# Kernel tuning notes

Measured on AMD Instinct MI355X. Metric: run time of the kernel, lower is better.

The kernel has to match this reference:

```python
import jax, jax.numpy as jnp
import numpy as np

N, D, E, TOP_K = 4096, 1024, 8, 2
NEG_INF = -1e38


def setup_inputs() -> dict:
    key = jax.random.key(0)
    ks = jax.random.split(key, 6)
    s = 1.0 / np.sqrt(D)
    return {
        "x": jax.random.normal(ks[0], (N, D), jnp.float32),
        "noise": jax.random.normal(ks[1], (E,), jnp.float32),
        "Wg": jax.random.normal(ks[2], (D, E), jnp.float32) * s,
        "Wn": jax.random.normal(ks[3], (D, E), jnp.float32) * s,
        "We": jax.random.normal(ks[4], (E, D, D), jnp.float32) * s,
        "be": jax.random.normal(ks[5], (E, D), jnp.float32) * 0.01,
    }


def reference(x, noise, Wg, Wn, We, be):
    # Gating: H = Wg(x) + randn(E) * softplus(Wnoise(x))   (Eq. 4-5)
    g = x @ Wg                                      # [N, E]
    H = g + noise[None, :] * jax.nn.softplus(x @ Wn)  # [N, E]
    # Keep top_k entries of H, set the rest to -Inf (scatter of bottom E-k)
    vals, idx = jax.lax.top_k(H, TOP_K)             # [N, k]
    keep = jnp.full_like(H, NEG_INF)
    keep = keep.at[jnp.arange(H.shape[0])[:, None], idx].set(vals)
    G = jax.nn.softmax(keep, axis=1)                # [N, E]; masked entries -> 0
    # Expert outputs; masked experts have G==0 so dense weighted sum matches
    # the sparse per-example loop: out_n = sum_j G[n,j] * expert_j(x_n)
    Y = jnp.einsum('nd,edh->neh', x, We) + be[None, :, :]  # [N, E, D]
    out = jnp.einsum('ne,neh->nh', G, Y)            # [N, D]
    return out
```

## Files before the change

### kernel.cpp

```cpp
#include <hip/hip_runtime.h>
#include <hip/hip_bf16.h>
#include <stdint.h>

#define NR   4096
#define DIM  1024
#define NE   8
#define BM   64
#define BN   128
#define BK   64

typedef __attribute__((ext_vector_type(8))) short  bf16x8;
typedef __attribute__((ext_vector_type(8))) ushort u16x8;
typedef __attribute__((ext_vector_type(4))) float  f32x4;

__device__ __forceinline__ ushort f2bf(float f) {
    union { __hip_bfloat16 h; ushort u; } cv;
    cv.h = __float2bfloat16(f);
    return cv.u;
}

__device__ __forceinline__ void gload16(const void* g, void* l) {
    __builtin_amdgcn_global_load_lds(
        (const __attribute__((address_space(1))) unsigned int*)g,
        (__attribute__((address_space(3))) unsigned int*)l, 16, 0, 0);
}

__global__ __launch_bounds__(256)
void k1_prep(const float* __restrict__ Wg, const float* __restrict__ Wn,
             float* __restrict__ WT, float* __restrict__ out) {
    const int tid = threadIdx.x;
    if (blockIdx.x < 8) {
        const int k    = blockIdx.x * 128 + (tid >> 1);
        const int half = tid & 1;
        const float* src = half ? Wn : Wg;
        const float4* s4 = (const float4*)(src + (size_t)k * NE);
        float4 a = s4[0], b = s4[1];
        float* d = WT + (size_t)half * 8 * DIM;
        d[(size_t)0 * DIM + k] = a.x; d[(size_t)1 * DIM + k] = a.y;
        d[(size_t)2 * DIM + k] = a.z; d[(size_t)3 * DIM + k] = a.w;
        d[(size_t)4 * DIM + k] = b.x; d[(size_t)5 * DIM + k] = b.y;
        d[(size_t)6 * DIM + k] = b.z; d[(size_t)7 * DIM + k] = b.w;
    } else {
        const int vb = blockIdx.x - 8;
        float4 z = {0.f, 0.f, 0.f, 0.f};
        for (int i = vb * 256 + tid; i < NR * DIM / 4; i += 512 * 256)
            ((float4*)out)[i] = z;
    }
}

__global__ __launch_bounds__(256)
void k2_main(const float* __restrict__ We, ushort* __restrict__ WeT,
             const float* __restrict__ x, const float* __restrict__ noise,
             const float* __restrict__ WT, ushort* __restrict__ xbf,
             uint32_t* __restrict__ eid, float2* __restrict__ wpair) {
    __shared__ float smem[64 * 68];
    const int tid = threadIdx.x;
    if (blockIdx.x < 2048) {
        const int b  = blockIdx.x;
        const int e  = b >> 8, kt = (b >> 4) & 15, ct = b & 15;
        const float* src = We + ((size_t)e * DIM + (size_t)kt * 64) * DIM + ct * 64;
#pragma unroll
        for (int j = 0; j < 4; ++j) {
            int idx = tid + j * 256;
            int r = idx >> 4, c4 = idx & 15;
            *(float4*)&smem[r * 68 + c4 * 4] = *(const float4*)(src + (size_t)r * DIM + c4 * 4);
        }
        __syncthreads();
        ushort* dst = WeT + ((size_t)e * DIM + (size_t)ct * 64) * DIM + kt * 64;
#pragma unroll
        for (int j = 0; j < 2; ++j) {
            int u = tid + j * 256;
            int c = u >> 3, ch = u & 7;
            ushort tmp[8];
#pragma unroll
            for (int q = 0; q < 8; ++q) tmp[q] = f2bf(smem[(ch * 8 + q) * 68 + c]);
            *(u16x8*)(dst + (size_t)c * DIM + ch * 8) = *(u16x8*)tmp;
        }
    } else {
        const int w = tid >> 6, l = tid & 63;
        const int row = (blockIdx.x - 2048) * 4 + w;
        const float* xr = x + (size_t)row * DIM;

        float4 xv[4];
#pragma unroll
        for (int q = 0; q < 4; ++q) xv[q] = *(const float4*)(xr + q * 256 + l * 4);
#pragma unroll
        for (int q = 0; q < 4; ++q) {
            ushort4 xb;
            xb.x = f2bf(xv[q].x); xb.y = f2bf(xv[q].y);
            xb.z = f2bf(xv[q].z); xb.w = f2bf(xv[q].w);
            *(ushort4*)(xbf + (size_t)row * DIM + q * 256 + l * 4) = xb;
        }

        float acc[16];
#pragma unroll
        for (int u = 0; u < 16; ++u) {
            const float* wr_ = WT + (size_t)u * DIM + l * 4;
            float s = 0.f;
#pragma unroll
            for (int q = 0; q < 4; ++q) {
                float4 wv = *(const float4*)(wr_ + q * 256);
                s += xv[q].x * wv.x + xv[q].y * wv.y + xv[q].z * wv.z + xv[q].w * wv.w;
            }
            acc[u] = s;
        }
#pragma unroll
        for (int u = 0; u < 16; ++u) smem[(w * 64 + l) * 17 + u] = acc[u];
        asm volatile("s_waitcnt lgkmcnt(0)" ::: "memory");
        const int c = l >> 4, u = l & 15;
        float v = 0.f;
#pragma unroll
        for (int i = 0; i < 16; ++i) v += smem[(w * 64 + c * 16 + i) * 17 + u];
        v += __shfl_xor(v, 16, 64);
        v += __shfl_xor(v, 32, 64);

        const int e = l & 7;
        float ag = __shfl(v, e, 64);
        float an = __shfl(v, e + 8, 64);
        float sp = (an > 0.f) ? (an + log1pf(expf(-an))) : log1pf(expf(an));
        float H  = ag + noise[e] * sp;

        float Hh[8];
#pragma unroll
        for (int k = 0; k < 8; ++k) Hh[k] = __shfl(H, k, 64);
        if (l == 0) {
            int e0 = 0; float v0 = Hh[0];
#pragma unroll
            for (int k = 1; k < 8; ++k) if (Hh[k] > v0) { v0 = Hh[k]; e0 = k; }
            int e1 = -1; float v1 = 0.f;
#pragma unroll
            for (int k = 0; k < 8; ++k)
                if (k != e0 && (e1 < 0 || Hh[k] > v1)) { v1 = Hh[k]; e1 = k; }
            float rr = expf(v1 - v0);
            float w0 = 1.f / (1.f + rr), w1 = 1.f - w0;
            eid[row] = (uint32_t)e0 | ((uint32_t)e1 << 8);
            float2 wp; wp.x = w0; wp.y = w1;
            wpair[row] = wp;
        }
    }
}

__global__ __launch_bounds__(1024)
void bucket_build(const uint32_t* __restrict__ eid, const float2* __restrict__ wpair,
                  int* __restrict__ cnt, int* __restrict__ idxl, float* __restrict__ wl) {
    const int bucket = blockIdx.x;
    const int slot = bucket >> 3, ex = bucket & 7;
    __shared__ int base;
    __shared__ int wsum[16];
    if (threadIdx.x == 0) base = 0;
    const int wid = threadIdx.x >> 6, lane = threadIdx.x & 63;
    int* bidx = idxl + (size_t)bucket * NR;
    float* bwl = wl + (size_t)bucket * NR;

    for (int c0 = 0; c0 < NR; c0 += 1024) {
        const int row = c0 + threadIdx.x;
        const uint32_t em = eid[row];
        const int e = slot ? (int)((em >> 8) & 255u) : (int)(em & 255u);
        const bool m = (e == ex);
        const unsigned long long bal = __ballot(m);
        if (lane == 0) wsum[wid] = __popcll(bal);
        __syncthreads();
        int wbase = base;
        for (int i = 0; i < wid; ++i) wbase += wsum[i];
        const int pos = wbase + __popcll(bal & ((1ull << lane) - 1ull));
        if (m) {
            bidx[pos] = row;
            float2 wp = wpair[row];
            bwl[pos]  = slot ? wp.y : wp.x;
        }
        __syncthreads();
        if (threadIdx.x == 0) {
            int s = 0;
#pragma unroll
            for (int i = 0; i < 16; ++i) s += wsum[i];
            base += s;
        }
        __syncthreads();
    }
    if (threadIdx.x == 0) cnt[bucket] = base;
}

__global__ __launch_bounds__(256, 3)
void moe_gemm(const ushort* __restrict__ xbf, const ushort* __restrict__ WeT,
              const float* __restrict__ be, const int* __restrict__ cnt,
              const int* __restrict__ idxl, const float* __restrict__ wl,
              float* __restrict__ out) {
    __shared__ ushort Al[2][BM][BK];
    __shared__ ushort Bl[2][BN][BK];

    const int q8 = gridDim.x >> 3;
    const int W  = (blockIdx.x & 7) * q8 + (blockIdx.x >> 3);
    const int item = W >> 3, cT = W & 7;

    int bucket = -1, tile = 0, accp = 0;
#pragma unroll
    for (int b = 0; b < 16; ++b) {
        int t = (cnt[b] + BM - 1) >> 6;
        if (bucket < 0 && item < accp + t) { bucket = b; tile = item - accp; }
        accp += t;
    }
    if (bucket < 0) return;
    const int count  = cnt[bucket];
    const int nrowsv = min(BM, count - tile * BM);
    const int e  = bucket & 7;
    const int c0 = cT * BN;
    const int*   rows = idxl + (size_t)bucket * NR + tile * BM;
    const float* wrow = wl   + (size_t)bucket * NR + tile * BM;

    const int tid = threadIdx.x, wid = tid >> 6, lane = tid & 63;
    const int wr = (wid >> 1) * 32, wc = (wid & 1) * 64;
    const int l16 = lane & 15, lhi = lane >> 4;

    const int schunk = ((lane & 7) ^ ((lane >> 3) & 7)) * 8;
    const ushort* aptr[2];
    const ushort* bptr[4];
#pragma unroll
    for (int q = 0; q < 2; ++q) {
        int r = q * 32 + wid * 8 + (lane >> 3);
        aptr[q] = xbf + (size_t)rows[min(r, nrowsv - 1)] * DIM + schunk;
    }
#pragma unroll
    for (int q = 0; q < 4; ++q) {
        int c = c0 + q * 32 + wid * 8 + (lane >> 3);
        bptr[q] = WeT + ((size_t)(e * DIM + c)) * DIM + schunk;
    }

    f32x4 acc[2][4];
#pragma unroll
    for (int m = 0; m < 2; ++m)
#pragma unroll
        for (int n = 0; n < 4; ++n) { f32x4 z = {0.f, 0.f, 0.f, 0.f}; acc[m][n] = z; }

#pragma unroll
    for (int q = 0; q < 2; ++q) gload16(aptr[q], &Al[0][q * 32 + wid * 8][0]);
#pragma unroll
    for (int q = 0; q < 4; ++q) gload16(bptr[q], &Bl[0][q * 32 + wid * 8][0]);

    const int NSTEP = DIM / BK;
    for (int s = 0; s < NSTEP; ++s) {
        const int buf = s & 1;
        if (s + 1 < NSTEP) {
            const int nb = buf ^ 1, k0 = (s + 1) * BK;
#pragma unroll
            for (int q = 0; q < 2; ++q) gload16(aptr[q] + k0, &Al[nb][q * 32 + wid * 8][0]);
#pragma unroll
            for (int q = 0; q < 4; ++q) gload16(bptr[q] + k0, &Bl[nb][q * 32 + wid * 8][0]);
            asm volatile("s_waitcnt vmcnt(6)" ::: "memory");
        } else {
            asm volatile("s_waitcnt vmcnt(0)" ::: "memory");
        }
        __builtin_amdgcn_s_barrier();

#pragma unroll
        for (int h = 0; h < 2; ++h) {
            const int slot = ((h * 4 + lhi) ^ (l16 & 7)) * 8;
            bf16x8 af[2], bfr[4];
#pragma unroll
            for (int m = 0; m < 2; ++m)
                af[m] = *(const bf16x8*)(&Al[buf][wr + m * 16 + l16][0] + slot);
#pragma unroll
            for (int n = 0; n < 4; ++n)
                bfr[n] = *(const bf16x8*)(&Bl[buf][wc + n * 16 + l16][0] + slot);
#pragma unroll
            for (int m = 0; m < 2; ++m)
#pragma unroll
                for (int n = 0; n < 4; ++n)
                    acc[m][n] = __builtin_amdgcn_mfma_f32_16x16x32_bf16(af[m], bfr[n], acc[m][n], 0, 0, 0);
        }
        asm volatile("s_waitcnt lgkmcnt(0)" ::: "memory");
        __builtin_amdgcn_s_barrier();
    }

    float bev[4];
#pragma unroll
    for (int n = 0; n < 4; ++n) bev[n] = be[(size_t)e * DIM + c0 + wc + n * 16 + l16];
#pragma unroll
    for (int m = 0; m < 2; ++m) {
#pragma unroll
        for (int r = 0; r < 4; ++r) {
            int rl = wr + m * 16 + lhi * 4 + r;
            if (rl < nrowsv) {
                int   gr = rows[rl];
                float w  = wrow[rl];
                float* op = out + (size_t)gr * DIM + c0 + wc;
#pragma unroll
                for (int n = 0; n < 4; ++n)
                    atomicAdd(&op[n * 16 + l16], w * (acc[m][n][r] + bev[n]));
            }
        }
    }
}

extern "C" void kernel_launch(void* const* d_in, const int* in_sizes, int n_in,
                              void* d_out, int out_size, void* d_ws, size_t ws_size,
                              hipStream_t stream) {
    const float* x     = (const float*)d_in[0];
    const float* noise = (const float*)d_in[1];
    const float* Wg    = (const float*)d_in[2];
    const float* Wn    = (const float*)d_in[3];
    const float* We    = (const float*)d_in[4];
    const float* be    = (const float*)d_in[5];
    float* out = (float*)d_out;

    char* w = (char*)d_ws;
    size_t off = 256;
    int*      cnt   = (int*)w;
    int*      idxl  = (int*)(w + off);      off += (size_t)2 * NE * NR * 4;
    float*    wl    = (float*)(w + off);    off += (size_t)2 * NE * NR * 4;
    uint32_t* eid   = (uint32_t*)(w + off); off += (size_t)NR * 4;
    float2*   wpair = (float2*)(w + off);   off += (size_t)NR * 8;
    off = (off + 255) & ~(size_t)255;
    float*  WT  = (float*)(w + off);  off += (size_t)16 * DIM * 4;
    ushort* xbf = (ushort*)(w + off); off += (size_t)NR * DIM * 2;
    ushort* WeT = (ushort*)(w + off); off += (size_t)NE * DIM * DIM * 2;

    k1_prep<<<520, 256, 0, stream>>>(Wg, Wn, WT, out);
    k2_main<<<3072, 256, 0, stream>>>(We, WeT, x, noise, WT, xbf, eid, wpair);
    bucket_build<<<16, 1024, 0, stream>>>(eid, wpair, cnt, idxl, wl);
    moe_gemm<<<144 * 8, 256, 0, stream>>>(xbf, WeT, be, cnt, idxl, wl, out);
}
```

Baseline: 87.05 us.

## Merge top-k slot buckets per expert and enlarge MoE GEMM row tiles

The top-1 and top-2 row lists are now built into one bucket per expert instead of one per (slot, expert) pair, which cuts the number of buckets and the padding in partially filled tiles. The grouped GEMM moves from 64-row tiles with 256 threads to 256-row tiles with 512 threads, using 96 KB of dynamic LDS and a 4x4 MFMA accumulator grid per wave. The aim is more reuse of each expert's weight tile per load and fewer redundant weight reads. In exchange the grid drops to about 320 blocks at one block per CU, which risks poor load balance and less latency hiding on a 256-CU part.

Result: slower. 97.71 us (+12.3%).

```diff
diff --git a/kernel.cpp b/kernel.cpp
--- a/kernel.cpp
+++ b/kernel.cpp
@@ -5,9 +5,12 @@
 #define NR   4096
 #define DIM  1024
 #define NE   8
-#define BM   64
+#define BM   256
 #define BN   128
-#define BK   64
+#define GBK  64
+#define LDSA (BM * GBK)
+#define LDSB (BN * GBK)
+#define LSLOT (LDSA + LDSB)
 
 typedef __attribute__((ext_vector_type(8))) short  bf16x8;
 typedef __attribute__((ext_vector_type(8))) ushort u16x8;
@@ -143,20 +146,20 @@
 __global__ __launch_bounds__(1024)
 void bucket_build(const uint32_t* __restrict__ eid, const float2* __restrict__ wpair,
                   int* __restrict__ cnt, int* __restrict__ idxl, float* __restrict__ wl) {
-    const int bucket = blockIdx.x;
-    const int slot = bucket >> 3, ex = bucket & 7;
+    const int ex = blockIdx.x;
     __shared__ int base;
     __shared__ int wsum[16];
     if (threadIdx.x == 0) base = 0;
     const int wid = threadIdx.x >> 6, lane = threadIdx.x & 63;
-    int* bidx = idxl + (size_t)bucket * NR;
-    float* bwl = wl + (size_t)bucket * NR;
+    int* bidx = idxl + (size_t)ex * NR;
+    float* bwl = wl + (size_t)ex * NR;
 
     for (int c0 = 0; c0 < NR; c0 += 1024) {
         const int row = c0 + threadIdx.x;
         const uint32_t em = eid[row];
-        const int e = slot ? (int)((em >> 8) & 255u) : (int)(em & 255u);
-        const bool m = (e == ex);
+        const bool m0 = (int)(em & 255u) == ex;
+        const bool m1 = (int)((em >> 8) & 255u) == ex;
+        const bool m = m0 || m1;
         const unsigned long long bal = __ballot(m);
         if (lane == 0) wsum[wid] = __popcll(bal);
         __syncthreads();
@@ -166,7 +169,7 @@
         if (m) {
             bidx[pos] = row;
             float2 wp = wpair[row];
-            bwl[pos]  = slot ? wp.y : wp.x;
+            bwl[pos]  = m0 ? wp.x : wp.y;
         }
         __syncthreads();
         if (threadIdx.x == 0) {
@@ -177,16 +180,15 @@
         }
         __syncthreads();
     }
-    if (threadIdx.x == 0) cnt[bucket] = base;
-}
-
-__global__ __launch_bounds__(256, 3)
+    if (threadIdx.x == 0) cnt[ex] = base;
+}
+
+__global__ __launch_bounds__(512, 1)
 void moe_gemm(const ushort* __restrict__ xbf, const ushort* __restrict__ WeT,
               const float* __restrict__ be, const int* __restrict__ cnt,
               const int* __restrict__ idxl, const float* __restrict__ wl,
               float* __restrict__ out) {
-    __shared__ ushort Al[2][BM][BK];
-    __shared__ ushort Bl[2][BN][BK];
+    extern __shared__ ushort lds[];
 
     const int q8 = gridDim.x >> 3;
     const int W  = (blockIdx.x & 7) * q8 + (blockIdx.x >> 3);
@@ -194,75 +196,83 @@
 
     int bucket = -1, tile = 0, accp = 0;
 #pragma unroll
-    for (int b = 0; b < 16; ++b) {
-        int t = (cnt[b] + BM - 1) >> 6;
+    for (int b = 0; b < NE; ++b) {
+        int t = (cnt[b] + BM - 1) >> 8;
         if (bucket < 0 && item < accp + t) { bucket = b; tile = item - accp; }
         accp += t;
     }
     if (bucket < 0) return;
     const int count  = cnt[bucket];
-    const int nrowsv = min(BM, count - tile * BM);
-    const int e  = bucket & 7;
+    const int nrows  = min(BM, count - tile * BM);
+    const int e  = bucket;
     const int c0 = cT * BN;
     const int*   rows = idxl + (size_t)bucket * NR + tile * BM;
     const float* wrow = wl   + (size_t)bucket * NR + tile * BM;
 
     const int tid = threadIdx.x, wid = tid >> 6, lane = tid & 63;
-    const int wr = (wid >> 1) * 32, wc = (wid & 1) * 64;
+    const int wr = (wid >> 1) * 64, wc = (wid & 1) * 64;
     const int l16 = lane & 15, lhi = lane >> 4;
-
-    const int schunk = ((lane & 7) ^ ((lane >> 3) & 7)) * 8;
-    const ushort* aptr[2];
-    const ushort* bptr[4];
+    const int lr8 = lane >> 3, lc8 = lane & 7;
+    const int chunkp = lc8 ^ lr8;
+
+    const ushort* aptr[4];
+    const ushort* bptr[2];
+#pragma unroll
+    for (int q = 0; q < 4; ++q) {
+        int r  = wid * 32 + q * 8 + lr8;
+        int gr = rows[min(r, nrows - 1)];
+        aptr[q] = xbf + (size_t)gr * DIM + chunkp * 8;
+    }
 #pragma unroll
     for (int q = 0; q < 2; ++q) {
-        int r = q * 32 + wid * 8 + (lane >> 3);
-        aptr[q] = xbf + (size_t)rows[min(r, nrowsv - 1)] * DIM + schunk;
-    }
-#pragma unroll
-    for (int q = 0; q < 4; ++q) {
-        int c = c0 + q * 32 + wid * 8 + (lane >> 3);
-        bptr[q] = WeT + ((size_t)(e * DIM + c)) * DIM + schunk;
-    }
-
-    f32x4 acc[2][4];
-#pragma unroll
-    for (int m = 0; m < 2; ++m)
+        int c = c0 + wid * 16 + q * 8 + lr8;
+        bptr[q] = WeT + ((size_t)(e * DIM + c)) * DIM + chunkp * 8;
+    }
+
+    f32x4 acc[4][4];
+#pragma unroll
+    for (int m = 0; m < 4; ++m)
 #pragma unroll
         for (int n = 0; n < 4; ++n) { f32x4 z = {0.f, 0.f, 0.f, 0.f}; acc[m][n] = z; }
 
-#pragma unroll
-    for (int q = 0; q < 2; ++q) gload16(aptr[q], &Al[0][q * 32 + wid * 8][0]);
-#pragma unroll
-    for (int q = 0; q < 4; ++q) gload16(bptr[q], &Bl[0][q * 32 + wid * 8][0]);
-
-    const int NSTEP = DIM / BK;
-    for (int s = 0; s < NSTEP; ++s) {
+#define STAGE(T, BUF) do {                                                     \
+    const int _k0 = (T) * GBK;                                                 \
+    ushort* _a = lds + (BUF) * LSLOT;                                          \
+    ushort* _bb = _a + LDSA;                                                   \
+    _Pragma("unroll")                                                          \
+    for (int q = 0; q < 4; ++q)                                                \
+        gload16(aptr[q] + _k0, _a + (wid * 32 + q * 8) * GBK);                 \
+    _Pragma("unroll")                                                          \
+    for (int q = 0; q < 2; ++q)                                                \
+        gload16(bptr[q] + _k0, _bb + (wid * 16 + q * 8) * GBK);                \
+} while (0)
+
+    const int NS = DIM / GBK;
+    STAGE(0, 0);
+    for (int s = 0; s < NS; ++s) {
         const int buf = s & 1;
-        if (s + 1 < NSTEP) {
-            const int nb = buf ^ 1, k0 = (s + 1) * BK;
-#pragma unroll
-            for (int q = 0; q < 2; ++q) gload16(aptr[q] + k0, &Al[nb][q * 32 + wid * 8][0]);
-#pragma unroll
-            for (int q = 0; q < 4; ++q) gload16(bptr[q] + k0, &Bl[nb][q * 32 + wid * 8][0]);
+        if (s + 1 < NS) {
+            STAGE(s + 1, buf ^ 1);
             asm volatile("s_waitcnt vmcnt(6)" ::: "memory");
         } else {
             asm volatile("s_waitcnt vmcnt(0)" ::: "memory");
         }
         __builtin_amdgcn_s_barrier();
 
+        const ushort* Ab = lds + buf * LSLOT;
+        const ushort* Bb = Ab + LDSA;
 #pragma unroll
         for (int h = 0; h < 2; ++h) {
-            const int slot = ((h * 4 + lhi) ^ (l16 & 7)) * 8;
-            bf16x8 af[2], bfr[4];
-#pragma unroll
-            for (int m = 0; m < 2; ++m)
-                af[m] = *(const bf16x8*)(&Al[buf][wr + m * 16 + l16][0] + slot);
+            bf16x8 af[4], bfr[4];
+            const int chb = (h * 4 + lhi) ^ (l16 & 7);
+#pragma unroll
+            for (int m = 0; m < 4; ++m)
+                af[m] = *(const bf16x8*)(Ab + (wr + m * 16 + l16) * GBK + chb * 8);
 #pragma unroll
             for (int n = 0; n < 4; ++n)
-                bfr[n] = *(const bf16x8*)(&Bl[buf][wc + n * 16 + l16][0] + slot);
-#pragma unroll
-            for (int m = 0; m < 2; ++m)
+                bfr[n] = *(const bf16x8*)(Bb + (wc + n * 16 + l16) * GBK + chb * 8);
+#pragma unroll
+            for (int m = 0; m < 4; ++m)
 #pragma unroll
                 for (int n = 0; n < 4; ++n)
                     acc[m][n] = __builtin_amdgcn_mfma_f32_16x16x32_bf16(af[m], bfr[n], acc[m][n], 0, 0, 0);
@@ -270,16 +280,17 @@
         asm volatile("s_waitcnt lgkmcnt(0)" ::: "memory");
         __builtin_amdgcn_s_barrier();
     }
+#undef STAGE
 
     float bev[4];
 #pragma unroll
     for (int n = 0; n < 4; ++n) bev[n] = be[(size_t)e * DIM + c0 + wc + n * 16 + l16];
 #pragma unroll
-    for (int m = 0; m < 2; ++m) {
+    for (int m = 0; m < 4; ++m) {
 #pragma unroll
         for (int r = 0; r < 4; ++r) {
             int rl = wr + m * 16 + lhi * 4 + r;
-            if (rl < nrowsv) {
+            if (rl < nrows) {
                 int   gr = rows[rl];
                 float w  = wrow[rl];
                 float* op = out + (size_t)gr * DIM + c0 + wc;
@@ -305,8 +316,8 @@
     char* w = (char*)d_ws;
     size_t off = 256;
     int*      cnt   = (int*)w;
-    int*      idxl  = (int*)(w + off);      off += (size_t)2 * NE * NR * 4;
-    float*    wl    = (float*)(w + off);    off += (size_t)2 * NE * NR * 4;
+    int*      idxl  = (int*)(w + off);      off += (size_t)NE * NR * 4;
+    float*    wl    = (float*)(w + off);    off += (size_t)NE * NR * 4;
     uint32_t* eid   = (uint32_t*)(w + off); off += (size_t)NR * 4;
     float2*   wpair = (float2*)(w + off);   off += (size_t)NR * 8;
     off = (off + 255) & ~(size_t)255;
@@ -314,8 +325,12 @@
     ushort* xbf = (ushort*)(w + off); off += (size_t)NR * DIM * 2;
     ushort* WeT = (ushort*)(w + off); off += (size_t)NE * DIM * DIM * 2;
 
+    (void)hipFuncSetAttribute((const void*)moe_gemm,
+                              hipFuncAttributeMaxDynamicSharedMemorySize,
+                              2 * LSLOT * (int)sizeof(ushort));
+
     k1_prep<<<520, 256, 0, stream>>>(Wg, Wn, WT, out);
     k2_main<<<3072, 256, 0, stream>>>(We, WeT, x, noise, WT, xbf, eid, wpair);
-    bucket_build<<<16, 1024, 0, stream>>>(eid, wpair, cnt, idxl, wl);
-    moe_gemm<<<144 * 8, 256, 0, stream>>>(xbf, WeT, be, cnt, idxl, wl, out);
-}
+    bucket_build<<<NE, 1024, 0, stream>>>(eid, wpair, cnt, idxl, wl);
+    moe_gemm<<<40 * 8, 512, 2 * LSLOT * sizeof(ushort), stream>>>(xbf, WeT, be, cnt, idxl, wl, out);
+}
```
